# Optimization experiments

Measured on AMD Instinct MI355X. Metric: run time of the kernel, lower is better.

The kernel has to match this reference:

```python
import jax, jax.numpy as jnp
import numpy as np
import math

HID, NH, DH = 512, 4, 128
H, W = 30, 54
N = H * W          # 1620 tokens
MEM, B = 2, 1
NG = 4             # temporal groups
L = (H // 2) * (W // 2)  # 405
FF = 4 * HID


def _ln(x, g, b, eps=1e-5):
    m = x.mean(-1, keepdims=True)
    v = ((x - m) ** 2).mean(-1, keepdims=True)
    return (x - m) / jnp.sqrt(v + eps) * g + b


def setup_inputs() -> dict:
    key = jax.random.key(0)
    ks = jax.random.split(key, 24)
    w = lambda k, s: (jax.random.normal(k, s, jnp.float32) * 0.02)
    return {
        'x': jax.random.normal(ks[0], (B, N, HID), jnp.float32),
        'memory': jax.random.normal(ks[1], (MEM, N, HID), jnp.float32),
        # spatial block params (weights stored as (in, out) so y = x @ W + b)
        's_g1': jnp.ones(HID), 's_b1': jnp.zeros(HID),
        's_wq': w(ks[2], (HID, HID)), 's_bq': jnp.zeros(HID),
        's_wk': w(ks[3], (HID, HID)), 's_bk': jnp.zeros(HID),
        's_wv': w(ks[4], (HID, HID)), 's_bv': jnp.zeros(HID),
        's_wo': w(ks[5], (HID, HID)), 's_bo': jnp.zeros(HID),
        's_g2': jnp.ones(HID), 's_b2': jnp.zeros(HID),
        's_w1': w(ks[6], (HID, FF)), 's_fb1': jnp.zeros(FF),
        's_w2': w(ks[7], (FF, HID)), 's_fb2': jnp.zeros(HID),
        # temporal block params (forward only uses norm2 + ffn)
        't_g2': jnp.ones(HID), 't_b2': jnp.zeros(HID),
        't_w1': w(ks[8], (HID, FF)), 't_fb1': jnp.zeros(FF),
        't_w2': w(ks[9], (FF, HID)), 't_fb2': jnp.zeros(HID),
    }


def _spatial_block(x, memory, g1, b1, wq, bq, wk, bk, wv, bv, wo, bo, g2, b2, w1, fb1, w2, fb2):
    xc = jnp.concatenate([x, memory], axis=0)          # (t, n, hid), t = B + MEM
    t = xc.shape[0]
    xn = _ln(xc, g1, b1)
    q = (xn @ wq + bq).reshape(t, N, NH, DH).transpose(0, 2, 1, 3)
    k = (xn @ wk + bk).reshape(t, N, NH, DH).transpose(0, 2, 1, 3)
    v = (xn @ wv + bv).reshape(t, N, NH, DH).transpose(0, 2, 1, 3)
    scores = jnp.einsum('thqd,thkd->thqk', q, k) / math.sqrt(DH)
    probs = jax.nn.softmax(scores, axis=-1)
    o = jnp.einsum('thqk,thkd->thqd', probs, v).transpose(0, 2, 1, 3).reshape(t, N, HID)
    o = o @ wo + bo
    xu = xc + o
    y = _ln(xu, g2, b2)
    xa = xu + (jax.nn.relu(y @ w1 + fb1) @ w2 + fb2)
    return xa[:B], jnp.concatenate([memory[1:], x], axis=0)


def _temporal_block(x, memory, g2, b2, w1, fb1, w2, fb2):
    xc = jnp.concatenate([x, memory], axis=0)          # (t, n, hid)
    t = xc.shape[0]
    # (t, 2, h/2, 2, w/2, NH, DH) -> (t, 2, 2, NH, h/2, w/2, DH) -> (t, NG, NH, L, DH)
    xg = xc.reshape(t, 2, H // 2, 2, W // 2, NH, DH)
    xg = xg.transpose(0, 1, 3, 5, 2, 4, 6).reshape(t, NG, NH, L, DH)
    # Original code runs SDPA over all t but keeps only slice [-1]; since Q is
    # broadcast across t, attn_out[-1] == attention(Q, K[-1], V[-1]) exactly.
    q = xg[-1]                                          # (NG, NH, L, DH); K = V = q
    scores = jnp.einsum('gnld,gnmd->gnlm', q, q) / math.sqrt(DH)
    probs = jax.nn.softmax(scores, axis=-1)
    o = jnp.einsum('gnlm,gnmd->gnld', probs, q)         # (NG, NH, L, DH)
    o = o.transpose(0, 2, 1, 3).reshape(NG, L, HID)
    o = o.mean(axis=0, keepdims=True)                   # (1, L, HID)
    x_att = jnp.tile(o, (1, NG, 1))                     # (1, n, HID)
    xu = x + x_att
    y = _ln(xu, g2, b2)
    x_fin = xu + (jax.nn.relu(y @ w1 + fb1) @ w2 + fb2)
    return x_fin, jnp.concatenate([memory[1:], x], axis=0)


def reference(x, memory, s_g1, s_b1, s_wq, s_bq, s_wk, s_bk, s_wv, s_bv, s_wo, s_bo,
              s_g2, s_b2, s_w1, s_fb1, s_w2, s_fb2, t_g2, t_b2, t_w1, t_fb1, t_w2, t_fb2):
    x_sp, mem_sp = _spatial_block(x, memory, s_g1, s_b1, s_wq, s_bq, s_wk, s_bk,
                                  s_wv, s_bv, s_wo, s_bo, s_g2, s_b2, s_w1, s_fb1, s_w2, s_fb2)
    x_fin, mem_fin = _temporal_block(x_sp, mem_sp, t_g2, t_b2, t_w1, t_fb1, t_w2, t_fb2)
    return x_fin, mem_fin
```

## Files before the change

### kernel.cpp

```cpp
#include <hip/hip_runtime.h>
#include <stdint.h>

typedef unsigned short u16;
typedef float f32x4 __attribute__((ext_vector_type(4)));
typedef short s16x8 __attribute__((ext_vector_type(8)));

#define DEV __device__ __forceinline__

DEV float b2f(u16 u){ union{unsigned i; float f;} v; v.i = ((unsigned)u)<<16; return v.f; }
DEV u16 f2b(float f){ union{float f; unsigned i;} v; v.f=f; unsigned u=v.i;
                      return (u16)((u + 0x7FFFu + ((u>>16)&1u))>>16); }
DEV s16x8 ld8(const u16* p){ return *(const s16x8*)p; }

#define MFMA(d,a,b) d = __builtin_amdgcn_mfma_f32_16x16x32_bf16(a, b, d, 0, 0, 0)

DEV void gload16(const u16* g, u16* l){
  __builtin_amdgcn_global_load_lds((const __attribute__((address_space(1))) void*)g,
                                   (__attribute__((address_space(3))) void*)l, 16, 0, 0);
}

__global__ __launch_bounds__(64) void detect_kernel(const u16* __restrict__ x, int* flag){
  int lane = threadIdx.x;
  int cnt = 0;
  for (int i=0;i<32;i++){
    u16 v = x[lane*32+i];
    int e = (v >> 7) & 0xFF;
    if (e >= 0xE0) cnt++;
  }
  for (int off=1; off<64; off<<=1) cnt += __shfl_xor(cnt, off, 64);
  if (lane==0) *flag = (cnt >= 16) ? 1 : 0;
}

struct NormArgs { const void* src[23]; int cumblk[24]; };

__global__ __launch_bounds__(64) void norm_kernel(NormArgs a, const int* __restrict__ flag,
                                                  u16* __restrict__ canon){
  int b = blockIdx.x, lane = threadIdx.x;
  int t = 0;
  while (t < 22 && b >= a.cumblk[t+1]) t++;
  int off = (b - a.cumblk[t])*512 + lane*8;
  size_t g = (size_t)b*512 + lane*8;
  if (*flag){
    const float* s = (const float*)a.src[t] + off;
    s16x8 o;
#pragma unroll
    for (int j=0;j<8;j++) o[j] = (short)f2b(s[j]);
    *(s16x8*)(canon+g) = o;
  } else {
    *(s16x8*)(canon+g) = *(const s16x8*)((const u16*)a.src[t] + off);
  }
}

struct TJobs {
  const u16* src[8]; u16* dst[8];
  int R[8], C32[8], srcld[8], dstld[8];
  int cum[9];
};
__global__ void trans_kernel(TJobs J){
  int b = blockIdx.x;
  int t = 0;
  while (b >= J.cum[t+1]) t++;
  int idx = b - J.cum[t];
  int tr = idx / J.C32[t], tc = idx - tr*J.C32[t];
  int r0 = tr*32, c0 = tc*32;
  const u16* src = J.src[t];
  u16* dst = J.dst[t];
  int R = J.R[t], srcld = J.srcld[t], dstld = J.dstld[t];
  __shared__ u16 tile[32][33];
  int tx = threadIdx.x, ty = threadIdx.y;
#pragma unroll
  for (int i=0;i<4;i++){
    int r = r0 + ty + i*8, c = c0 + tx;
    u16 v = 0;
    if (r < R) v = src[(size_t)r*srcld + c];
    tile[ty+i*8][tx] = v;
  }
  __syncthreads();
#pragma unroll
  for (int i=0;i<4;i++){
    int c = c0 + ty + i*8, r = r0 + tx;
    if (r < dstld) dst[(size_t)c*dstld + r] = tile[tx][ty+i*8];
  }
}

__global__ __launch_bounds__(256) void gemm_s_kernel(
    const u16* __restrict__ A, const u16* __restrict__ BT,
    const u16* __restrict__ bias, const u16* __restrict__ bias2, const u16* __restrict__ bias3,
    int M, int N, int K, int KS, float* __restrict__ pout,
    const u16* __restrict__ resid_bf, const float* __restrict__ resid_f,
    u16* __restrict__ out_bf, float* __restrict__ out_f,
    const int* __restrict__ flagp, u16* __restrict__ dev_bf, float* __restrict__ dev_f,
    int relu)
{
  __shared__ u16 Al[2][64*64];
  __shared__ u16 Bl[2][64*64];
  int tid = threadIdx.x, lane = tid & 63, w = tid >> 6;
  int lr = lane & 15, lk = lane >> 4;
  int wr = w >> 1, wc = w & 1;
  int rowBase = blockIdx.y*64, colBase = blockIdx.x*64;
  int z = blockIdx.z;
  int kStep = K / KS;
  int kOff = kStep * z;
  int nk = kStep >> 6;

  f32x4 acc[2][2] = {{{0,0,0,0},{0,0,0,0}},{{0,0,0,0},{0,0,0,0}}};

  auto STAGE = [&](int buf, int kt){
    int kb = kOff + kt*64;
#pragma unroll
    for (int it=0; it<2; ++it){
      int ch  = it*256 + tid;
      int row = ch >> 3, seg = ch & 7;
      int sseg = (seg ^ (row & 7)) << 3;
      int ar = min(rowBase + row, M-1);
      gload16(A  + (size_t)ar*K + kb + sseg, Al[buf] + ch*8);
      int bc = colBase + row;
      gload16(BT + (size_t)bc*K + kb + sseg, Bl[buf] + ch*8);
    }
  };

  STAGE(0, 0);
  asm volatile("s_waitcnt vmcnt(0)" ::: "memory");
  __syncthreads();
  int cur = 0;
  for (int kt=0; kt<nk; ++kt){
    if (kt+1 < nk) STAGE(cur^1, kt+1);
#pragma unroll
    for (int ks=0; ks<2; ++ks){
      s16x8 af[2], bf[2];
#pragma unroll
      for (int m=0;m<2;m++){
        int ar = wr*32 + m*16 + lr;
        af[m] = *(const s16x8*)(Al[cur] + ar*64 + ((((ks<<2)+lk) ^ (ar&7))<<3));
        int bc = wc*32 + m*16 + lr;
        bf[m] = *(const s16x8*)(Bl[cur] + bc*64 + ((((ks<<2)+lk) ^ (bc&7))<<3));
      }
#pragma unroll
      for (int m=0;m<2;m++)
#pragma unroll
        for (int n=0;n<2;n++) MFMA(acc[m][n], af[m], bf[n]);
    }
    asm volatile("s_waitcnt vmcnt(0)" ::: "memory");
    __syncthreads();
    cur ^= 1;
  }

  if (pout){
    float* pz = pout + (size_t)z*M*N;
#pragma unroll
    for (int m=0;m<2;m++)
#pragma unroll
      for (int n=0;n<2;n++){
        int col = colBase + wc*32 + n*16 + lr;
#pragma unroll
        for (int r=0;r<4;r++){
          int row = rowBase + wr*32 + m*16 + lk*4 + r;
          if (row < M) pz[(size_t)row*N + col] = acc[m][n][r];
        }
      }
    return;
  }
  int isf32 = flagp ? *flagp : 0;
#pragma unroll
  for (int m=0;m<2;m++){
#pragma unroll
    for (int n=0;n<2;n++){
      int col = colBase + wc*32 + n*16 + lr;
      float bv = 0.f;
      if (bias){
        if (bias2){
          const u16* bp = (col < 512) ? bias : ((col < 1024) ? bias2 : bias3);
          bv = b2f(bp[col & 511]);
        } else bv = b2f(bias[col]);
      }
#pragma unroll
      for (int r=0;r<4;r++){
        int row = rowBase + wr*32 + m*16 + lk*4 + r;
        if (row < M){
          float v = acc[m][n][r] + bv;
          if (relu) v = fmaxf(v, 0.f);
          size_t idx = (size_t)row*N + col;
          if (resid_bf) v += b2f(resid_bf[idx]);
          if (resid_f)  v += resid_f[idx];
          if (out_f)  out_f[idx]  = v;
          if (out_bf) out_bf[idx] = f2b(v);
          if (flagp){ if (isf32) dev_f[idx] = v; else dev_bf[idx] = f2b(v); }
        }
      }
    }
  }
}

__global__ __launch_bounds__(256) void gemm_comb_kernel(
    const float* __restrict__ pout, int KS, const u16* __restrict__ bias,
    int M, int N, int relu,
    const u16* __restrict__ resid_bf, const float* __restrict__ resid_f,
    u16* __restrict__ out_bf, float* __restrict__ out_f,
    const int* __restrict__ flagp, u16* __restrict__ dev_bf, float* __restrict__ dev_f)
{
  int w = threadIdx.x >> 6, lane = threadIdx.x & 63;
  int row = blockIdx.x*4 + w;
  if (row >= M) return;
  int c0 = lane*8;
  float acc[8];
  const float* p0 = pout + (size_t)row*N + c0;
#pragma unroll
  for (int j=0;j<8;j++) acc[j] = p0[j];
  for (int z=1; z<KS; ++z){
    const float* pz = pout + ((size_t)z*M + row)*N + c0;
#pragma unroll
    for (int j=0;j<8;j++) acc[j] += pz[j];
  }
  int isf32 = flagp ? *flagp : 0;
#pragma unroll
  for (int j=0;j<8;j++){
    int col = c0 + j;
    float v = acc[j] + (bias ? b2f(bias[col]) : 0.f);
    if (relu) v = fmaxf(v, 0.f);
    size_t idx = (size_t)row*N + col;
    if (resid_bf) v += b2f(resid_bf[idx]);
    if (resid_f)  v += resid_f[idx];
    if (out_f)  out_f[idx]  = v;
    if (out_bf) out_bf[idx] = f2b(v);
    if (flagp){ if (isf32) dev_f[idx] = v; else dev_bf[idx] = f2b(v); }
  }
}

__global__ __launch_bounds__(256) void flash4_kernel(
    const u16* __restrict__ Qp, const u16* __restrict__ Kp, const u16* __restrict__ VTp,
    float* __restrict__ po, float* __restrict__ pm, float* __restrict__ pl,
    int M, int Nk, int qld, int tiles_total, int nchunks,
    long q_hi_stride, long vt_hi_stride, int vt_ld, float scale)
{
  int u = blockIdx.y, c = blockIdx.z;
  int uh = u >> 2, ul = u & 3;
  const u16* q  = Qp  + (size_t)uh*q_hi_stride + ul*128;
  const u16* kk = Kp  + (size_t)uh*q_hi_stride + ul*128;
  const u16* vt = VTp + (size_t)uh*vt_hi_stride + (size_t)(ul*128)*vt_ld;
  int tid = threadIdx.x, lane = tid & 63, w = tid >> 6;
  int lr = lane & 15, lk = lane >> 4;
  int r0 = blockIdx.x*64 + w*16;
  int qr = min(r0 + lr, M-1);

  __shared__ u16 Klds[64*128];
  __shared__ u16 Vlds[128*64];
  __shared__ u16 plsm[4][16*80];

  s16x8 qf[4];
#pragma unroll
  for (int kd=0; kd<4; ++kd) qf[kd] = ld8(q + (size_t)qr*qld + kd*32 + lk*8);
  f32x4 oacc[8];
#pragma unroll
  for (int i=0;i<8;i++) oacc[i] = (f32x4){0,0,0,0};
  float mr[4] = {-1e30f,-1e30f,-1e30f,-1e30f};
  float ls[4] = {0,0,0,0};

  int t0 = (tiles_total * c) / nchunks;
  int t1 = (tiles_total * (c+1)) / nchunks;
  for (int kt=t0; kt<t1; ++kt){
    int kb = kt*64;
#pragma unroll
    for (int it=0; it<4; ++it){
      int ch = it*256 + tid;
      int key = ch >> 4, seg = ch & 15;
      int kg = min(kb + key, Nk-1);
      s16x8 kvv = ld8(kk + (size_t)kg*qld + seg*8);
      int dd = ch >> 3, sg = ch & 7;
      s16x8 vvv = ld8(vt + (size_t)dd*vt_ld + kb + sg*8);
      *(s16x8*)(Klds + key*128 + ((seg*8) ^ ((key&7)<<3))) = kvv;
      *(s16x8*)(Vlds + dd*64  + ((sg*8)  ^ ((dd&7)<<3)))  = vvv;
    }
    __syncthreads();
    f32x4 s[4];
#pragma unroll
    for (int n=0;n<4;n++) s[n] = (f32x4){0,0,0,0};
#pragma unroll
    for (int n=0;n<4;n++){
      int key = n*16 + lr;
#pragma unroll
      for (int kd=0; kd<4; ++kd){
        s16x8 kf = *(const s16x8*)(Klds + key*128 + ((kd*32 + lk*8) ^ ((key&7)<<3)));
        MFMA(s[n], qf[kd], kf);
      }
    }
#pragma unroll
    for (int n=0;n<4;n++){
      bool valid = (kb + n*16 + lr) < Nk;
#pragma unroll
      for (int r=0;r<4;r++){
        float v2 = s[n][r]*scale;
        s[n][r] = valid ? v2 : -1e30f;
      }
    }
    float mx[4];
#pragma unroll
    for (int r=0;r<4;r++) mx[r] = fmaxf(fmaxf(s[0][r],s[1][r]), fmaxf(s[2][r],s[3][r]));
#pragma unroll
    for (int off=1; off<16; off<<=1){
#pragma unroll
      for (int r=0;r<4;r++) mx[r] = fmaxf(mx[r], __shfl_xor(mx[r], off, 64));
    }
    float al[4], rs[4];
#pragma unroll
    for (int r=0;r<4;r++){
      float mnew = fmaxf(mr[r], mx[r]);
      al[r] = __expf(mr[r]-mnew);
      mr[r] = mnew;
      rs[r] = 0.f;
    }
#pragma unroll
    for (int n=0;n<4;n++){
#pragma unroll
      for (int r=0;r<4;r++){
        float p = __expf(s[n][r]-mr[r]);
        rs[r] += p;
        plsm[w][(lk*4+r)*80 + n*16 + lr] = f2b(p);
      }
    }
#pragma unroll
    for (int off=1; off<16; off<<=1){
#pragma unroll
      for (int r=0;r<4;r++) rs[r] += __shfl_xor(rs[r], off, 64);
    }
#pragma unroll
    for (int r=0;r<4;r++) ls[r] = ls[r]*al[r] + rs[r];
#pragma unroll
    for (int cf=0; cf<8; cf++){
#pragma unroll
      for (int r=0;r<4;r++) oacc[cf][r] *= al[r];
    }
    __syncthreads();
#pragma unroll
    for (int kd2=0; kd2<2; ++kd2){
      s16x8 pa = *(const s16x8*)(plsm[w] + lr*80 + kd2*32 + lk*8);
#pragma unroll
      for (int cf=0; cf<8; ++cf){
        int dd = cf*16 + lr;
        s16x8 vb = *(const s16x8*)(Vlds + dd*64 + ((kd2*32 + lk*8) ^ ((dd&7)<<3)));
        MFMA(oacc[cf], pa, vb);
      }
    }
    __syncthreads();
  }
  size_t pbase = ((size_t)u*nchunks + c)*M;
#pragma unroll
  for (int cf=0; cf<8; ++cf){
#pragma unroll
    for (int r=0;r<4;r++){
      int row = r0 + lk*4 + r;
      if (row < M) po[(pbase + row)*128 + cf*16 + lr] = oacc[cf][r];
    }
  }
  if (lr == 0){
#pragma unroll
    for (int r=0;r<4;r++){
      int row = r0 + lk*4 + r;
      if (row < M){ pm[pbase + row] = mr[r]; pl[pbase + row] = ls[r]; }
    }
  }
}

__global__ __launch_bounds__(256) void fcomb_kernel(
    const float* __restrict__ po, const float* __restrict__ pm, const float* __restrict__ pl,
    u16* __restrict__ out_bf, float* __restrict__ out_f,
    int rows, int nunits, int nchunks, long o_hi_stride)
{
  int w = threadIdx.x >> 6, lane = threadIdx.x & 63;
  int gid = blockIdx.x*4 + w;
  if (gid >= nunits*rows) return;
  int u = gid / rows, row = gid - u*rows;
  size_t pb = (size_t)u*nchunks*rows + row;
  float m = -1e30f;
  for (int c=0;c<nchunks;c++) m = fmaxf(m, pm[pb + (size_t)c*rows]);
  float L = 0.f, o0 = 0.f, o1 = 0.f;
  for (int c=0;c<nchunks;c++){
    float wgt = __expf(pm[pb + (size_t)c*rows] - m);
    L += wgt * pl[pb + (size_t)c*rows];
    const float* op = po + (pb + (size_t)c*rows)*128;
    o0 += wgt * op[lane*2];
    o1 += wgt * op[lane*2+1];
  }
  float inv = 1.f/L;
  int uh = u>>2, ul = u&3;
  size_t idx = (size_t)uh*o_hi_stride + (size_t)row*512 + ul*128 + lane*2;
  if (out_bf){ out_bf[idx] = f2b(o0*inv); out_bf[idx+1] = f2b(o1*inv); }
  else       { out_f[idx]  = o0*inv;      out_f[idx+1]  = o1*inv; }
}

__global__ __launch_bounds__(256) void ln_kernel(
    const u16* __restrict__ inb, const float* __restrict__ inf,
    const u16* __restrict__ gw, const u16* __restrict__ bw,
    u16* __restrict__ out, int rows)
{
  int w = threadIdx.x >> 6, lane = threadIdx.x & 63;
  int row = blockIdx.x*4 + w;
  if (row >= rows) return;
  float x[8];
  if (inb){
    s16x8 v = ld8(inb + (size_t)row*512 + lane*8);
#pragma unroll
    for (int j=0;j<8;j++) x[j] = b2f((u16)v[j]);
  } else {
    const float* p = inf + (size_t)row*512 + lane*8;
#pragma unroll
    for (int j=0;j<8;j++) x[j] = p[j];
  }
  float s = 0.f;
#pragma unroll
  for (int j=0;j<8;j++) s += x[j];
#pragma unroll
  for (int off=1; off<64; off<<=1) s += __shfl_xor(s, off, 64);
  float mean = s*(1.f/512.f);
  float vs = 0.f;
#pragma unroll
  for (int j=0;j<8;j++){ float d = x[j]-mean; vs += d*d; }
#pragma unroll
  for (int off=1; off<64; off<<=1) vs += __shfl_xor(vs, off, 64);
  float rstd = 1.f/sqrtf(vs*(1.f/512.f) + 1e-5f);
#pragma unroll
  for (int j=0;j<8;j++){
    int c = lane*8+j;
    float y = (x[j]-mean)*rstd*b2f(gw[c]) + b2f(bw[c]);
    out[(size_t)row*512 + c] = f2b(y);
  }
}

__global__ __launch_bounds__(256) void gather_xg_kernel(const u16* __restrict__ x,
                                                        u16* __restrict__ xg)
{
  int w = threadIdx.x >> 6, lane = threadIdx.x & 63;
  int gl = blockIdx.x*4 + w;
  int g = gl/405, l = gl - g*405;
  int a = g >> 1, b = g & 1, hh = l/27, ww = l - hh*27;
  int n = a*810 + hh*54 + b*27 + ww;
  *(s16x8*)(xg + (size_t)gl*512 + lane*8) = *(const s16x8*)(x + (size_t)n*512 + lane*8);
}

__global__ __launch_bounds__(256) void combine_kernel(const float* __restrict__ xa0,
                                                      const float* __restrict__ ot,
                                                      float* __restrict__ xut)
{
  int w = threadIdx.x >> 6, lane = threadIdx.x & 63;
  int row = blockIdx.x*4 + w;
  int l = row % 405;
  int c = lane*8;
  const float* pa = xa0 + (size_t)row*512 + c;
  float acc[8];
#pragma unroll
  for (int j=0;j<8;j++) acc[j] = pa[j];
#pragma unroll
  for (int g2=0; g2<4; ++g2){
    const float* po = ot + ((size_t)(g2*405+l))*512 + c;
#pragma unroll
    for (int j=0;j<8;j++) acc[j] += 0.25f*po[j];
  }
  float* pw = xut + (size_t)row*512 + c;
#pragma unroll
  for (int j=0;j<8;j++) pw[j] = acc[j];
}

__global__ __launch_bounds__(256) void copy_out_kernel(
    const u16* __restrict__ s16, const float* __restrict__ s32,
    const int* __restrict__ flag, u16* __restrict__ dbf, float* __restrict__ df, int n8)
{
  int i = blockIdx.x*256 + threadIdx.x;
  if (i >= n8) return;
  if (*flag){
    ((f32x4*)df)[i*2]   = ((const f32x4*)s32)[i*2];
    ((f32x4*)df)[i*2+1] = ((const f32x4*)s32)[i*2+1];
  } else {
    ((s16x8*)dbf)[i] = ((const s16x8*)s16)[i];
  }
}

extern "C" void kernel_launch(void* const* d_in, const int* in_sizes, int n_in,
                              void* d_out, int out_size, void* d_ws, size_t ws_size,
                              hipStream_t stream)
{
  u16* outp16 = (u16*)d_out;
  float* outp32 = (float*)d_out;

  char* wsb = (char*)d_ws;
  size_t off = 0;
  auto alloc = [&](size_t bytes)->void*{
    void* p = wsb + off; off += (bytes + 255) & ~(size_t)255; return p; };

  int* flagp = (int*)alloc(256);

  static const int din_idx[23] = {0, 2,3, 4,5, 6,7, 8,9, 10,11, 12,13,
                                  14,15, 16,17, 18,19, 20,21, 22,23};
  static const int din_n[23]   = {829440, 512,512, 262144,512, 262144,512,
                                  262144,512, 262144,512, 512,512,
                                  1048576,2048, 1048576,512, 512,512,
                                  1048576,2048, 1048576,512};
  NormArgs na;
  u16* cptr[23];
  int total = 0;
  for (int i=0;i<23;i++){ na.src[i] = d_in[din_idx[i]]; na.cumblk[i] = total/512; total += din_n[i]; }
  na.cumblk[23] = total/512;
  u16* canon = (u16*)alloc((size_t)total*2);
  { int c = 0; for (int i=0;i<23;i++){ cptr[i] = canon + c; c += din_n[i]; } }
  const u16 *cx=cptr[0], *cg1=cptr[1], *cb1=cptr[2],
            *cwq=cptr[3], *cbq=cptr[4], *cwk=cptr[5], *cbk=cptr[6],
            *cwv=cptr[7], *cbv=cptr[8], *cwo=cptr[9], *cbo=cptr[10],
            *cg2=cptr[11], *cb2=cptr[12], *cw1s=cptr[13], *cfb1s=cptr[14],
            *cw2s=cptr[15], *cfb2s=cptr[16], *ctg2=cptr[17], *ctb2=cptr[18],
            *cw1t=cptr[19], *cfb1t=cptr[20], *cw2t=cptr[21], *cfb2t=cptr[22];

  u16* wqkvT = (u16*)alloc((size_t)1536*512*2);
  u16* woT  = (u16*)alloc(512*512*2);
  u16* w1sT = (u16*)alloc(2048*512*2);
  u16* w2sT = (u16*)alloc((size_t)512*2048*2);
  u16* w1tT = (u16*)alloc(2048*512*2);
  u16* w2tT = (u16*)alloc((size_t)512*2048*2);
  u16* xn   = (u16*)alloc(1620*512*2);
  u16* qkv  = (u16*)alloc((size_t)1620*1536*2);
  u16* vT   = (u16*)alloc((size_t)512*1664*2);
  u16* attn = (u16*)alloc(1620*512*2);
  float* xu = (float*)alloc((size_t)1620*512*4);
  u16* yb   = (u16*)alloc(1620*512*2);
  u16* hh   = (u16*)alloc((size_t)1620*2048*2);
  float* xa0= (float*)alloc((size_t)1620*512*4);
  u16* xg   = (u16*)alloc(1620*512*2);
  u16* xgT  = (u16*)alloc((size_t)4*512*448*2);
  float* ot = (float*)alloc((size_t)4*405*512*4);
  float* xut= (float*)alloc((size_t)1620*512*4);
  u16* yt   = (u16*)alloc(1620*512*2);
  u16* ht   = (u16*)alloc((size_t)1620*2048*2);
  float* po = (float*)alloc((size_t)4*8*1620*128*4);
  float* pm = (float*)alloc((size_t)4*8*1620*4);
  float* pl = (float*)alloc((size_t)4*8*1620*4);

  const float scale = 0.08838834764831843f;
  dim3 tb(32,8);

  detect_kernel<<<dim3(1), dim3(64), 0, stream>>>((const u16*)d_in[0], flagp);
  norm_kernel<<<dim3(total/512), dim3(64), 0, stream>>>(na, flagp, canon);

  {
    TJobs J;
    const u16* srcs[8] = {cwq, cwk, cwv, cwo, cw1s, cw2s, cw1t, cw2t};
    u16* dsts[8] = {wqkvT, wqkvT + (size_t)512*512, wqkvT + (size_t)1024*512,
                    woT, w1sT, w2sT, w1tT, w2tT};
    int Rs[8]   = {512,512,512,512, 512,2048, 512,2048};
    int Cs[8]   = {512,512,512,512, 2048,512, 2048,512};
    int t2 = 0;
    J.cum[0] = 0;
    for (int i=0;i<8;i++){
      J.src[i]=srcs[i]; J.dst[i]=dsts[i]; J.R[i]=Rs[i]; J.C32[i]=Cs[i]/32;
      J.srcld[i]=Cs[i]; J.dstld[i]=Rs[i];
      t2 += (Rs[i]/32)*(Cs[i]/32);
      J.cum[i+1]=t2;
    }
    trans_kernel<<<dim3(t2), tb, 0, stream>>>(J);
  }

  ln_kernel<<<dim3(405), dim3(256), 0, stream>>>(cx, nullptr, cg1, cb1, xn, 1620);
  gemm_s_kernel<<<dim3(24,26,1), dim3(256), 0, stream>>>(xn, wqkvT, cbq, cbk, cbv,
      1620,1536,512, 1, nullptr, nullptr,nullptr, qkv, nullptr, nullptr,nullptr,nullptr, 0);
  {
    TJobs J;
    J.src[0]=qkv+1024; J.dst[0]=vT; J.R[0]=1620; J.C32[0]=512/32;
    J.srcld[0]=1536; J.dstld[0]=1664;
    int t2 = (1664/32)*(512/32);
    J.cum[0]=0; for (int i=1;i<9;i++) J.cum[i]=t2;
    trans_kernel<<<dim3(t2), tb, 0, stream>>>(J);
  }
  flash4_kernel<<<dim3(26,4,8), dim3(256), 0, stream>>>(qkv, qkv+512, vT, po, pm, pl,
      1620, 1620, 1536, 26, 8, 0L, 0L, 1664, scale);
  fcomb_kernel<<<dim3(1620), dim3(256), 0, stream>>>(po, pm, pl, attn, nullptr,
      1620, 4, 8, 0L);
  gemm_s_kernel<<<dim3(8,26,2), dim3(256), 0, stream>>>(attn, woT, nullptr,nullptr,nullptr,
      1620,512,512, 2, po, nullptr,nullptr, nullptr,nullptr, nullptr,nullptr,nullptr, 0);
  gemm_comb_kernel<<<dim3(405), dim3(256), 0, stream>>>(po, 2, cbo, 1620,512, 0,
      cx, nullptr, nullptr, xu, nullptr,nullptr,nullptr);
  ln_kernel<<<dim3(405), dim3(256), 0, stream>>>(nullptr, xu, cg2, cb2, yb, 1620);
  gemm_s_kernel<<<dim3(32,26,1), dim3(256), 0, stream>>>(yb, w1sT, cfb1s, nullptr,nullptr,
      1620,2048,512, 1, nullptr, nullptr,nullptr, hh, nullptr, nullptr,nullptr,nullptr, 1);
  gemm_s_kernel<<<dim3(8,26,2), dim3(256), 0, stream>>>(hh, w2sT, nullptr,nullptr,nullptr,
      1620,512,2048, 2, po, nullptr,nullptr, nullptr,nullptr, nullptr,nullptr,nullptr, 0);
  gemm_comb_kernel<<<dim3(405), dim3(256), 0, stream>>>(po, 2, cfb2s, 1620,512, 0,
      nullptr, xu, nullptr, xa0, flagp, outp16 + 1658880, outp32 + 1658880);

  gather_xg_kernel<<<dim3(405), dim3(256), 0, stream>>>(cx, xg);
  {
    TJobs J;
    int per = (448/32)*(512/32);
    for (int g=0; g<4; ++g){
      J.src[g]=xg + (size_t)g*405*512; J.dst[g]=xgT + (size_t)g*512*448;
      J.R[g]=405; J.C32[g]=512/32; J.srcld[g]=512; J.dstld[g]=448;
    }
    J.cum[0]=0;
    for (int i=1;i<9;i++) J.cum[i] = (i<=4) ? per*i : per*4;
    trans_kernel<<<dim3(per*4), tb, 0, stream>>>(J);
  }
  flash4_kernel<<<dim3(7,16,7), dim3(256), 0, stream>>>(xg, xg, xgT, po, pm, pl,
      405, 405, 512, 7, 7, (long)(405*512), (long)(512*448), 448, scale);
  fcomb_kernel<<<dim3(1620), dim3(256), 0, stream>>>(po, pm, pl, nullptr, ot,
      405, 16, 7, (long)(405*512));
  combine_kernel<<<dim3(405), dim3(256), 0, stream>>>(xa0, ot, xut);
  ln_kernel<<<dim3(405), dim3(256), 0, stream>>>(nullptr, xut, ctg2, ctb2, yt, 1620);
  gemm_s_kernel<<<dim3(32,26,1), dim3(256), 0, stream>>>(yt, w1tT, cfb1t, nullptr,nullptr,
      1620,2048,512, 1, nullptr, nullptr,nullptr, ht, nullptr, nullptr,nullptr,nullptr, 1);
  gemm_s_kernel<<<dim3(8,26,2), dim3(256), 0, stream>>>(ht, w2tT, nullptr,nullptr,nullptr,
      1620,512,2048, 2, po, nullptr,nullptr, nullptr,nullptr, nullptr,nullptr,nullptr, 0);
  gemm_comb_kernel<<<dim3(405), dim3(256), 0, stream>>>(po, 2, cfb2t, 1620,512, 0,
      nullptr, xut, nullptr, nullptr, flagp, outp16, outp32);

  copy_out_kernel<<<dim3(405), dim3(256), 0, stream>>>((const u16*)d_in[0],
      (const float*)d_in[0], flagp, outp16 + 829440, outp32 + 829440, 103680);
}
```

Measured before the change: 308.3 us.

## Fuse residual-combine with LayerNorm, fold weight conversion into transpose, cut flash splits

Two LayerNorm passes are fused into the preceding split-K combine and temporal-combine kernels, so xu/xut are no longer re-read from memory by a separate LN kernel. Weight matrices are converted straight from the raw inputs inside the transpose kernel instead of first going through the canonical bf16 copy, which shrinks the normalisation pass. The flash-attention key splits drop from 8 and 7 to 4, and s_setprio hints are wrapped around the MFMA sections. The trade-off is fewer blocks for the attention kernels and a dtype branch in the transpose loads.

Result: faster. 281.8 us (-8.6%).

```diff
diff --git a/kernel.cpp b/kernel.cpp
--- a/kernel.cpp
+++ b/kernel.cpp
@@ -31,13 +31,13 @@
   if (lane==0) *flag = (cnt >= 16) ? 1 : 0;
 }
 
-struct NormArgs { const void* src[23]; int cumblk[24]; };
+struct NormArgs { const void* src[15]; int cumblk[16]; };
 
 __global__ __launch_bounds__(64) void norm_kernel(NormArgs a, const int* __restrict__ flag,
                                                   u16* __restrict__ canon){
   int b = blockIdx.x, lane = threadIdx.x;
   int t = 0;
-  while (t < 22 && b >= a.cumblk[t+1]) t++;
+  while (t < 14 && b >= a.cumblk[t+1]) t++;
   int off = (b - a.cumblk[t])*512 + lane*8;
   size_t g = (size_t)b*512 + lane*8;
   if (*flag){
@@ -52,27 +52,31 @@
 }
 
 struct TJobs {
-  const u16* src[8]; u16* dst[8];
+  const void* src[8]; u16* dst[8];
   int R[8], C32[8], srcld[8], dstld[8];
   int cum[9];
 };
-__global__ void trans_kernel(TJobs J){
+__global__ void trans_kernel(TJobs J, const int* __restrict__ flag){
   int b = blockIdx.x;
   int t = 0;
   while (b >= J.cum[t+1]) t++;
   int idx = b - J.cum[t];
   int tr = idx / J.C32[t], tc = idx - tr*J.C32[t];
   int r0 = tr*32, c0 = tc*32;
-  const u16* src = J.src[t];
+  const void* src = J.src[t];
   u16* dst = J.dst[t];
   int R = J.R[t], srcld = J.srcld[t], dstld = J.dstld[t];
+  int isf32 = flag ? *flag : 0;
   __shared__ u16 tile[32][33];
   int tx = threadIdx.x, ty = threadIdx.y;
 #pragma unroll
   for (int i=0;i<4;i++){
     int r = r0 + ty + i*8, c = c0 + tx;
     u16 v = 0;
-    if (r < R) v = src[(size_t)r*srcld + c];
+    if (r < R){
+      size_t si = (size_t)r*srcld + c;
+      v = isf32 ? f2b(((const float*)src)[si]) : ((const u16*)src)[si];
+    }
     tile[ty+i*8][tx] = v;
   }
   __syncthreads();
@@ -193,7 +197,7 @@
 
 __global__ __launch_bounds__(256) void gemm_comb_kernel(
     const float* __restrict__ pout, int KS, const u16* __restrict__ bias,
-    int M, int N, int relu,
+    int M, int relu,
     const u16* __restrict__ resid_bf, const float* __restrict__ resid_f,
     u16* __restrict__ out_bf, float* __restrict__ out_f,
     const int* __restrict__ flagp, u16* __restrict__ dev_bf, float* __restrict__ dev_f)
@@ -203,11 +207,11 @@
   if (row >= M) return;
   int c0 = lane*8;
   float acc[8];
-  const float* p0 = pout + (size_t)row*N + c0;
+  const float* p0 = pout + (size_t)row*512 + c0;
 #pragma unroll
   for (int j=0;j<8;j++) acc[j] = p0[j];
   for (int z=1; z<KS; ++z){
-    const float* pz = pout + ((size_t)z*M + row)*N + c0;
+    const float* pz = pout + ((size_t)z*M + row)*512 + c0;
 #pragma unroll
     for (int j=0;j<8;j++) acc[j] += pz[j];
   }
@@ -217,12 +221,94 @@
     int col = c0 + j;
     float v = acc[j] + (bias ? b2f(bias[col]) : 0.f);
     if (relu) v = fmaxf(v, 0.f);
-    size_t idx = (size_t)row*N + col;
+    size_t idx = (size_t)row*512 + col;
     if (resid_bf) v += b2f(resid_bf[idx]);
     if (resid_f)  v += resid_f[idx];
     if (out_f)  out_f[idx]  = v;
     if (out_bf) out_bf[idx] = f2b(v);
     if (flagp){ if (isf32) dev_f[idx] = v; else dev_bf[idx] = f2b(v); }
+  }
+}
+
+__global__ __launch_bounds__(256) void comb_ln_kernel(
+    const float* __restrict__ pout, int KS, const u16* __restrict__ bias, int M,
+    const u16* __restrict__ resid_bf,
+    float* __restrict__ out_f,
+    const u16* __restrict__ gw, const u16* __restrict__ bw,
+    u16* __restrict__ out_ln)
+{
+  int w = threadIdx.x >> 6, lane = threadIdx.x & 63;
+  int row = blockIdx.x*4 + w;
+  if (row >= M) return;
+  int c0 = lane*8;
+  float acc[8];
+  const float* p0 = pout + (size_t)row*512 + c0;
+#pragma unroll
+  for (int j=0;j<8;j++) acc[j] = p0[j];
+  for (int z=1; z<KS; ++z){
+    const float* pz = pout + ((size_t)z*M + row)*512 + c0;
+#pragma unroll
+    for (int j=0;j<8;j++) acc[j] += pz[j];
+  }
+  float s = 0.f;
+#pragma unroll
+  for (int j=0;j<8;j++){
+    acc[j] += b2f(bias[c0+j]) + b2f(resid_bf[(size_t)row*512 + c0 + j]);
+    out_f[(size_t)row*512 + c0 + j] = acc[j];
+    s += acc[j];
+  }
+#pragma unroll
+  for (int off=1; off<64; off<<=1) s += __shfl_xor(s, off, 64);
+  float mean = s*(1.f/512.f);
+  float vs = 0.f;
+#pragma unroll
+  for (int j=0;j<8;j++){ float d = acc[j]-mean; vs += d*d; }
+#pragma unroll
+  for (int off=1; off<64; off<<=1) vs += __shfl_xor(vs, off, 64);
+  float rstd = 1.f/sqrtf(vs*(1.f/512.f) + 1e-5f);
+#pragma unroll
+  for (int j=0;j<8;j++){
+    int c = c0+j;
+    out_ln[(size_t)row*512 + c] = f2b((acc[j]-mean)*rstd*b2f(gw[c]) + b2f(bw[c]));
+  }
+}
+
+__global__ __launch_bounds__(256) void combine_ln_kernel(
+    const float* __restrict__ xa0, const float* __restrict__ ot,
+    float* __restrict__ xut,
+    const u16* __restrict__ gw, const u16* __restrict__ bw,
+    u16* __restrict__ out_ln)
+{
+  int w = threadIdx.x >> 6, lane = threadIdx.x & 63;
+  int row = blockIdx.x*4 + w;
+  int l = row % 405;
+  int c0 = lane*8;
+  const float* pa = xa0 + (size_t)row*512 + c0;
+  float acc[8];
+#pragma unroll
+  for (int j=0;j<8;j++) acc[j] = pa[j];
+#pragma unroll
+  for (int g2=0; g2<4; ++g2){
+    const float* po = ot + ((size_t)(g2*405+l))*512 + c0;
+#pragma unroll
+    for (int j=0;j<8;j++) acc[j] += 0.25f*po[j];
+  }
+  float s = 0.f;
+#pragma unroll
+  for (int j=0;j<8;j++){ xut[(size_t)row*512 + c0 + j] = acc[j]; s += acc[j]; }
+#pragma unroll
+  for (int off=1; off<64; off<<=1) s += __shfl_xor(s, off, 64);
+  float mean = s*(1.f/512.f);
+  float vs = 0.f;
+#pragma unroll
+  for (int j=0;j<8;j++){ float d = acc[j]-mean; vs += d*d; }
+#pragma unroll
+  for (int off=1; off<64; off<<=1) vs += __shfl_xor(vs, off, 64);
+  float rstd = 1.f/sqrtf(vs*(1.f/512.f) + 1e-5f);
+#pragma unroll
+  for (int j=0;j<8;j++){
+    int c = c0+j;
+    out_ln[(size_t)row*512 + c] = f2b((acc[j]-mean)*rstd*b2f(gw[c]) + b2f(bw[c]));
   }
 }
 
@@ -274,6 +360,7 @@
     f32x4 s[4];
 #pragma unroll
     for (int n=0;n<4;n++) s[n] = (f32x4){0,0,0,0};
+    __builtin_amdgcn_s_setprio(1);
 #pragma unroll
     for (int n=0;n<4;n++){
       int key = n*16 + lr;
@@ -283,6 +370,7 @@
         MFMA(s[n], qf[kd], kf);
       }
     }
+    __builtin_amdgcn_s_setprio(0);
 #pragma unroll
     for (int n=0;n<4;n++){
       bool valid = (kb + n*16 + lr) < Nk;
@@ -330,6 +418,7 @@
       for (int r=0;r<4;r++) oacc[cf][r] *= al[r];
     }
     __syncthreads();
+    __builtin_amdgcn_s_setprio(1);
 #pragma unroll
     for (int kd2=0; kd2<2; ++kd2){
       s16x8 pa = *(const s16x8*)(plsm[w] + lr*80 + kd2*32 + lk*8);
@@ -340,6 +429,7 @@
         MFMA(oacc[cf], pa, vb);
       }
     }
+    __builtin_amdgcn_s_setprio(0);
     __syncthreads();
   }
   size_t pbase = ((size_t)u*nchunks + c)*M;
@@ -436,29 +526,6 @@
   *(s16x8*)(xg + (size_t)gl*512 + lane*8) = *(const s16x8*)(x + (size_t)n*512 + lane*8);
 }
 
-__global__ __launch_bounds__(256) void combine_kernel(const float* __restrict__ xa0,
-                                                      const float* __restrict__ ot,
-                                                      float* __restrict__ xut)
-{
-  int w = threadIdx.x >> 6, lane = threadIdx.x & 63;
-  int row = blockIdx.x*4 + w;
-  int l = row % 405;
-  int c = lane*8;
-  const float* pa = xa0 + (size_t)row*512 + c;
-  float acc[8];
-#pragma unroll
-  for (int j=0;j<8;j++) acc[j] = pa[j];
-#pragma unroll
-  for (int g2=0; g2<4; ++g2){
-    const float* po = ot + ((size_t)(g2*405+l))*512 + c;
-#pragma unroll
-    for (int j=0;j<8;j++) acc[j] += 0.25f*po[j];
-  }
-  float* pw = xut + (size_t)row*512 + c;
-#pragma unroll
-  for (int j=0;j<8;j++) pw[j] = acc[j];
-}
-
 __global__ __launch_bounds__(256) void copy_out_kernel(
     const u16* __restrict__ s16, const float* __restrict__ s32,
     const int* __restrict__ flag, u16* __restrict__ dbf, float* __restrict__ df, int n8)
@@ -487,25 +554,20 @@
 
   int* flagp = (int*)alloc(256);
 
-  static const int din_idx[23] = {0, 2,3, 4,5, 6,7, 8,9, 10,11, 12,13,
-                                  14,15, 16,17, 18,19, 20,21, 22,23};
-  static const int din_n[23]   = {829440, 512,512, 262144,512, 262144,512,
-                                  262144,512, 262144,512, 512,512,
-                                  1048576,2048, 1048576,512, 512,512,
-                                  1048576,2048, 1048576,512};
+  static const int din_idx[15] = {0, 2,3, 5,7,9,11, 12,13, 15,17, 18,19, 21,23};
+  static const int din_n[15]   = {829440, 512,512, 512,512,512,512, 512,512,
+                                  2048,512, 512,512, 2048,512};
   NormArgs na;
-  u16* cptr[23];
+  u16* cptr[15];
   int total = 0;
-  for (int i=0;i<23;i++){ na.src[i] = d_in[din_idx[i]]; na.cumblk[i] = total/512; total += din_n[i]; }
-  na.cumblk[23] = total/512;
+  for (int i=0;i<15;i++){ na.src[i] = d_in[din_idx[i]]; na.cumblk[i] = total/512; total += din_n[i]; }
+  na.cumblk[15] = total/512;
   u16* canon = (u16*)alloc((size_t)total*2);
-  { int c = 0; for (int i=0;i<23;i++){ cptr[i] = canon + c; c += din_n[i]; } }
+  { int c = 0; for (int i=0;i<15;i++){ cptr[i] = canon + c; c += din_n[i]; } }
   const u16 *cx=cptr[0], *cg1=cptr[1], *cb1=cptr[2],
-            *cwq=cptr[3], *cbq=cptr[4], *cwk=cptr[5], *cbk=cptr[6],
-            *cwv=cptr[7], *cbv=cptr[8], *cwo=cptr[9], *cbo=cptr[10],
-            *cg2=cptr[11], *cb2=cptr[12], *cw1s=cptr[13], *cfb1s=cptr[14],
-            *cw2s=cptr[15], *cfb2s=cptr[16], *ctg2=cptr[17], *ctb2=cptr[18],
-            *cw1t=cptr[19], *cfb1t=cptr[20], *cw2t=cptr[21], *cfb2t=cptr[22];
+            *cbq=cptr[3], *cbk=cptr[4], *cbv=cptr[5], *cbo=cptr[6],
+            *cg2=cptr[7], *cb2=cptr[8], *cfb1s=cptr[9], *cfb2s=cptr[10],
+            *ctg2=cptr[11], *ctb2=cptr[12], *cfb1t=cptr[13], *cfb2t=cptr[14];
 
   u16* wqkvT = (u16*)alloc((size_t)1536*512*2);
   u16* woT  = (u16*)alloc(512*512*2);
@@ -527,9 +589,9 @@
   float* xut= (float*)alloc((size_t)1620*512*4);
   u16* yt   = (u16*)alloc(1620*512*2);
   u16* ht   = (u16*)alloc((size_t)1620*2048*2);
-  float* po = (float*)alloc((size_t)4*8*1620*128*4);
-  float* pm = (float*)alloc((size_t)4*8*1620*4);
-  float* pl = (float*)alloc((size_t)4*8*1620*4);
+  float* po = (float*)alloc((size_t)4*4*1620*128*4);
+  float* pm = (float*)alloc((size_t)4*4*1620*4);
+  float* pl = (float*)alloc((size_t)4*4*1620*4);
 
   const float scale = 0.08838834764831843f;
   dim3 tb(32,8);
@@ -539,7 +601,8 @@
 
   {
     TJobs J;
-    const u16* srcs[8] = {cwq, cwk, cwv, cwo, cw1s, cw2s, cw1t, cw2t};
+    const void* srcs[8] = {d_in[4], d_in[6], d_in[8], d_in[10],
+                           d_in[14], d_in[16], d_in[20], d_in[22]};
     u16* dsts[8] = {wqkvT, wqkvT + (size_t)512*512, wqkvT + (size_t)1024*512,
                     woT, w1sT, w2sT, w1tT, w2tT};
     int Rs[8]   = {512,512,512,512, 512,2048, 512,2048};
@@ -552,7 +615,7 @@
       t2 += (Rs[i]/32)*(Cs[i]/32);
       J.cum[i+1]=t2;
     }
-    trans_kernel<<<dim3(t2), tb, 0, stream>>>(J);
+    trans_kernel<<<dim3(t2), tb, 0, stream>>>(J, flagp);
   }
 
   ln_kernel<<<dim3(405), dim3(256), 0, stream>>>(cx, nullptr, cg1, cb1, xn, 1620);
@@ -564,22 +627,21 @@
     J.srcld[0]=1536; J.dstld[0]=1664;
     int t2 = (1664/32)*(512/32);
     J.cum[0]=0; for (int i=1;i<9;i++) J.cum[i]=t2;
-    trans_kernel<<<dim3(t2), tb, 0, stream>>>(J);
-  }
-  flash4_kernel<<<dim3(26,4,8), dim3(256), 0, stream>>>(qkv, qkv+512, vT, po, pm, pl,
-      1620, 1620, 1536, 26, 8, 0L, 0L, 1664, scale);
+    trans_kernel<<<dim3(t2), tb, 0, stream>>>(J, nullptr);
+  }
+  flash4_kernel<<<dim3(26,4,4), dim3(256), 0, stream>>>(qkv, qkv+512, vT, po, pm, pl,
+      1620, 1620, 1536, 26, 4, 0L, 0L, 1664, scale);
   fcomb_kernel<<<dim3(1620), dim3(256), 0, stream>>>(po, pm, pl, attn, nullptr,
-      1620, 4, 8, 0L);
+      1620, 4, 4, 0L);
   gemm_s_kernel<<<dim3(8,26,2), dim3(256), 0, stream>>>(attn, woT, nullptr,nullptr,nullptr,
       1620,512,512, 2, po, nullptr,nullptr, nullptr,nullptr, nullptr,nullptr,nullptr, 0);
-  gemm_comb_kernel<<<dim3(405), dim3(256), 0, stream>>>(po, 2, cbo, 1620,512, 0,
-      cx, nullptr, nullptr, xu, nullptr,nullptr,nullptr);
-  ln_kernel<<<dim3(405), dim3(256), 0, stream>>>(nullptr, xu, cg2, cb2, yb, 1620);
+  comb_ln_kernel<<<dim3(405), dim3(256), 0, stream>>>(po, 2, cbo, 1620, cx, xu,
+      cg2, cb2, yb);
   gemm_s_kernel<<<dim3(32,26,1), dim3(256), 0, stream>>>(yb, w1sT, cfb1s, nullptr,nullptr,
       1620,2048,512, 1, nullptr, nullptr,nullptr, hh, nullptr, nullptr,nullptr,nullptr, 1);
   gemm_s_kernel<<<dim3(8,26,2), dim3(256), 0, stream>>>(hh, w2sT, nullptr,nullptr,nullptr,
       1620,512,2048, 2, po, nullptr,nullptr, nullptr,nullptr, nullptr,nullptr,nullptr, 0);
-  gemm_comb_kernel<<<dim3(405), dim3(256), 0, stream>>>(po, 2, cfb2s, 1620,512, 0,
+  gemm_comb_kernel<<<dim3(405), dim3(256), 0, stream>>>(po, 2, cfb2s, 1620, 0,
       nullptr, xu, nullptr, xa0, flagp, outp16 + 1658880, outp32 + 1658880);
 
   gather_xg_kernel<<<dim3(405), dim3(256), 0, stream>>>(cx, xg);
@@ -592,19 +654,18 @@
     }
     J.cum[0]=0;
     for (int i=1;i<9;i++) J.cum[i] = (i<=4) ? per*i : per*4;
-    trans_kernel<<<dim3(per*4), tb, 0, stream>>>(J);
-  }
-  flash4_kernel<<<dim3(7,16,7), dim3(256), 0, stream>>>(xg, xg, xgT, po, pm, pl,
-      405, 405, 512, 7, 7, (long)(405*512), (long)(512*448), 448, scale);
+    trans_kernel<<<dim3(per*4), tb, 0, stream>>>(J, nullptr);
+  }
+  flash4_kernel<<<dim3(7,16,4), dim3(256), 0, stream>>>(xg, xg, xgT, po, pm, pl,
+      405, 405, 512, 7, 4, (long)(405*512), (long)(512*448), 448, scale);
   fcomb_kernel<<<dim3(1620), dim3(256), 0, stream>>>(po, pm, pl, nullptr, ot,
-      405, 16, 7, (long)(405*512));
-  combine_kernel<<<dim3(405), dim3(256), 0, stream>>>(xa0, ot, xut);
-  ln_kernel<<<dim3(405), dim3(256), 0, stream>>>(nullptr, xut, ctg2, ctb2, yt, 1620);
+      405, 16, 4, (long)(405*512));
+  combine_ln_kernel<<<dim3(405), dim3(256), 0, stream>>>(xa0, ot, xut, ctg2, ctb2, yt);
   gemm_s_kernel<<<dim3(32,26,1), dim3(256), 0, stream>>>(yt, w1tT, cfb1t, nullptr,nullptr,
       1620,2048,512, 1, nullptr, nullptr,nullptr, ht, nullptr, nullptr,nullptr,nullptr, 1);
   gemm_s_kernel<<<dim3(8,26,2), dim3(256), 0, stream>>>(ht, w2tT, nullptr,nullptr,nullptr,
       1620,512,2048, 2, po, nullptr,nullptr, nullptr,nullptr, nullptr,nullptr,nullptr, 0);
-  gemm_comb_kernel<<<dim3(405), dim3(256), 0, stream>>>(po, 2, cfb2t, 1620,512, 0,
+  gemm_comb_kernel<<<dim3(405), dim3(256), 0, stream>>>(po, 2, cfb2t, 1620, 0,
       nullptr, xut, nullptr, nullptr, flagp, outp16, outp32);
 
   copy_out_kernel<<<dim3(405), dim3(256), 0, stream>>>((const u16*)d_in[0],
```
